# Kernel tuning notes

Hardware: AMD Instinct MI355X
Metric: run time of the kernel (lower is better)

## Reference

```python
import jax, jax.numpy as jnp
import numpy as np

N_NODES = 50000
N_EDGES = 800000
IN_DIM = 64
HID = 128
NUM_GRAPHS = 256


def setup_inputs() -> dict:
    key = jax.random.key(0)
    ks = jax.random.split(key, 20)
    inp = {
        'x': jax.random.normal(ks[0], (N_NODES, IN_DIM), dtype=jnp.float32),
        'edge_index': jax.random.randint(ks[1], (2, N_EDGES), 0, N_NODES, dtype=jnp.int32),
        'batch_idx': jnp.sort(jax.random.randint(ks[2], (N_NODES,), 0, NUM_GRAPHS, dtype=jnp.int32)),
    }
    # GIN layer MLP params (3 layers): Linear(in,hid)->ReLU->Linear(hid,hid)
    dims = [(IN_DIM, HID), (HID, HID), (HID, HID)]
    ki = 3
    for li, (di, dh) in enumerate(dims):
        s1 = 1.0 / np.sqrt(di)
        s2 = 1.0 / np.sqrt(dh)
        inp[f'gin{li}_w1'] = jax.random.uniform(ks[ki], (di, dh), jnp.float32, -s1, s1); ki += 1
        inp[f'gin{li}_b1'] = jnp.zeros((dh,), jnp.float32)
        inp[f'gin{li}_w2'] = jax.random.uniform(ks[ki], (dh, dh), jnp.float32, -s2, s2); ki += 1
        inp[f'gin{li}_b2'] = jnp.zeros((dh,), jnp.float32)
    # head: Linear(2*HID, HID) -> ReLU -> (Dropout eval=id) -> Linear(HID, 1)
    sh = 1.0 / np.sqrt(2 * HID)
    so = 1.0 / np.sqrt(HID)
    inp['head_w1'] = jax.random.uniform(ks[ki], (2 * HID, HID), jnp.float32, -sh, sh); ki += 1
    inp['head_b1'] = jnp.zeros((HID,), jnp.float32)
    inp['head_w2'] = jax.random.uniform(ks[ki], (HID, 1), jnp.float32, -so, so); ki += 1
    inp['head_b2'] = jnp.zeros((1,), jnp.float32)
    return inp


def _gin_layer(h, src, dst, w1, b1, w2, b2):
    # GINConv with eps=0: mlp(x + sum_{j->i} x_j), followed by outer ReLU
    agg = jax.ops.segment_sum(h[src], dst, num_segments=N_NODES)
    z = h + agg
    z = jnp.dot(jax.nn.relu(jnp.dot(z, w1) + b1), w2) + b2
    return jax.nn.relu(z)


def reference(x, edge_index, batch_idx,
              gin0_w1, gin0_b1, gin0_w2, gin0_b2,
              gin1_w1, gin1_b1, gin1_w2, gin1_b2,
              gin2_w1, gin2_b1, gin2_w2, gin2_b2,
              head_w1, head_b1, head_w2, head_b2):
    src, dst = edge_index[0], edge_index[1]
    h = _gin_layer(x, src, dst, gin0_w1, gin0_b1, gin0_w2, gin0_b2)
    h = _gin_layer(h, src, dst, gin1_w1, gin1_b1, gin1_w2, gin1_b2)
    h = _gin_layer(h, src, dst, gin2_w1, gin2_b1, gin2_w2, gin2_b2)
    # meanmax readout over graphs
    cnt = jax.ops.segment_sum(jnp.ones((h.shape[0],), h.dtype), batch_idx,
                              num_segments=NUM_GRAPHS)  # [G]
    ssum = jax.ops.segment_sum(h, batch_idx, num_segments=NUM_GRAPHS)  # [G, HID]
    mean_pool = ssum / jnp.maximum(cnt, 1.0)[:, None]
    max_pool = jax.ops.segment_max(h, batch_idx, num_segments=NUM_GRAPHS)
    max_pool = jnp.where(cnt[:, None] > 0, max_pool, 0.0)
    graph_repr = jnp.concatenate([mean_pool, max_pool], axis=-1)  # [G, 2*HID]
    # fraud head (dropout is identity in eval)
    hh = jax.nn.relu(jnp.dot(graph_repr, head_w1) + head_b1)
    logits = jnp.dot(hh, head_w2) + head_b2  # [G, 1]
    score = jax.nn.sigmoid(logits)
    return score
```

## Files before the change

kernel.cpp:

```cpp
#include <hip/hip_runtime.h>
#include <hip/hip_bf16.h>

#define N_NODES   50000
#define N_EDGES   800000
#define IN_DIM    64
#define HID       128
#define NUM_GRAPHS 256
#define NBUCK     196
#define BCAP      8192

typedef __bf16 bf16x8 __attribute__((ext_vector_type(8)));
typedef unsigned short u16x8 __attribute__((ext_vector_type(8)));
typedef float f32x4 __attribute__((ext_vector_type(4)));

__device__ __forceinline__ float b2f(unsigned short u) {
    return __uint_as_float(((unsigned int)u) << 16);
}
__device__ __forceinline__ unsigned short f2b(float f) {
    unsigned int x = __float_as_uint(f);
    x = (x + 0x7fffu + ((x >> 16) & 1u)) >> 16;
    return (unsigned short)x;
}

__global__ void diag_kernel(unsigned short* out, unsigned short pat) {
    out[threadIdx.x] = pat;
}

__global__ __launch_bounds__(256) void mega_pre_kernel(
    const unsigned short* __restrict__ x,
    const void* w0, const void* w1, const void* w2,
    const void* w3, const void* w4, const void* w5,
    unsigned short* __restrict__ wfbase,
    const int* __restrict__ batch, int* __restrict__ gstart,
    float* __restrict__ psum, unsigned int* __restrict__ pmax,
    const void* hw1, unsigned short* __restrict__ w1t,
    int* __restrict__ bcursor, int* __restrict__ flagp) {
    int b = blockIdx.x;
    int tid = threadIdx.x;

    if (b < 352) {
        __shared__ int cnt;
        if (tid == 0) cnt = 0;
        __syncthreads();
        unsigned short u = x[2 * tid];
        int e = (u >> 7) & 0xff;
        if (e <= 100 || e >= 140) atomicAdd(&cnt, 1);
        __syncthreads();
        int flag = cnt > 64;

        int mat, boff;
        if (b < 32) { mat = 0; boff = b; }
        else { mat = 1 + (b - 32) / 64; boff = (b - 32) % 64; }
        const void* W = mat == 0 ? w0 : mat == 1 ? w1 : mat == 2 ? w2
                      : mat == 3 ? w3 : mat == 4 ? w4 : w5;
        int KC = (mat == 0) ? 2 : 4;
        int idx = boff * 256 + tid;
        int j  = idx & 7;
        int l  = (idx >> 3) & 63;
        int tc = idx >> 9;
        int c  = tc % KC;
        int t  = tc / KC;
        int k  = c * 32 + (l >> 4) * 8 + j;
        int n  = t * 16 + (l & 15);
        unsigned short v = flag ? f2b(((const float*)W)[k * 128 + n])
                                : ((const unsigned short*)W)[k * 128 + n];
        wfbase[mat * 16384 + idx] = v;
    } else if (b < 548) {
        int i = (b - 352) * 256 + tid;
        if (i < NUM_GRAPHS * HID) { psum[i] = 0.0f; pmax[i] = 0u; }
        if (i >= N_NODES) return;
        int b1 = batch[i];
        int b0 = (i == 0) ? -1 : batch[i - 1];
        for (int g = b0 + 1; g <= b1; g++) gstart[g] = i;
        if (i == N_NODES - 1)
            for (int g = b1 + 1; g <= NUM_GRAPHS; g++) gstart[g] = N_NODES;
    } else if (b < 580) {
        __shared__ int cnt;
        if (tid == 0) cnt = 0;
        __syncthreads();
        unsigned short u = x[2 * tid];
        int e = (u >> 7) & 0xff;
        if (e <= 100 || e >= 140) atomicAdd(&cnt, 1);
        __syncthreads();
        int flag = cnt > 64;
        int base = (b - 548) * 1024;
#pragma unroll
        for (int j = 0; j < 4; j++) {
            int idx = base + j * 256 + tid;
            int n = idx >> 8;
            int k = idx & 255;
            unsigned short v = flag ? f2b(((const float*)hw1)[k * 128 + n])
                                    : ((const unsigned short*)hw1)[k * 128 + n];
            w1t[idx] = v;
        }
    } else {
        if (tid < NBUCK) bcursor[tid] = tid * BCAP;
        __shared__ int cnt;
        if (tid == 0) cnt = 0;
        __syncthreads();
        int c = 0;
        for (int j = 0; j < 16; j++) {
            unsigned short u = x[2 * (tid * 16 + j)];
            int e = (u >> 7) & 0xff;
            if (e <= 100 || e >= 140) c++;
        }
        atomicAdd(&cnt, c);
        __syncthreads();
        if (tid == 0) *flagp = (cnt > 1024) ? 1 : 0;
    }
}

__global__ __launch_bounds__(1024) void bscatter_kernel(const int* __restrict__ src,
        const int* __restrict__ dst, int* __restrict__ bcursor,
        unsigned int* __restrict__ ebuf) {
    __shared__ int lcnt[NBUCK];
    __shared__ int lbase[NBUCK];
    __shared__ int lcur[NBUCK];
    int tid = threadIdx.x;
    if (tid < NBUCK) lcnt[tid] = 0;
    __syncthreads();
    int e0 = blockIdx.x * 4096;
    int d[4], s[4];
#pragma unroll
    for (int k = 0; k < 4; k++) {
        int e = e0 + k * 1024 + tid;
        if (e < N_EDGES) {
            d[k] = dst[e]; s[k] = src[e];
            atomicAdd(&lcnt[d[k] >> 8], 1);
        } else d[k] = -1;
    }
    __syncthreads();
    if (tid < NBUCK) {
        int c = lcnt[tid];
        lbase[tid] = c ? atomicAdd(&bcursor[tid], c) : 0;
        lcur[tid] = 0;
    }
    __syncthreads();
#pragma unroll
    for (int k = 0; k < 4; k++) {
        if (d[k] >= 0) {
            int b = d[k] >> 8;
            int p = lbase[b] + atomicAdd(&lcur[b], 1);
            ebuf[p] = ((unsigned int)(d[k] & 255) << 16) | (unsigned int)s[k];
        }
    }
}

__global__ __launch_bounds__(256) void bsort_kernel(const unsigned int* __restrict__ ebuf,
        const int* __restrict__ bcursor, int* __restrict__ off,
        unsigned short* __restrict__ csr) {
    __shared__ int cntA[256];
    __shared__ int sc[256];
    __shared__ int lcnt[256];
    __shared__ int lcur[256];
    int b = blockIdx.x, tid = threadIdx.x;

    int v = (tid < NBUCK) ? (bcursor[tid] - tid * BCAP) : 0;
    cntA[tid] = v;
    sc[tid] = v;
    __syncthreads();
    for (int d = 1; d < 256; d <<= 1) {
        int t = (tid >= d) ? sc[tid - d] : 0;
        __syncthreads();
        sc[tid] += t;
        __syncthreads();
    }
    int base = sc[b] - cntA[b];
    int cnt  = cntA[b];
    int ebase = b * BCAP;
    __syncthreads();

    lcnt[tid] = 0;
    __syncthreads();
    for (int i = tid; i < cnt; i += 256)
        atomicAdd(&lcnt[ebuf[ebase + i] >> 16], 1);
    __syncthreads();
    int v2 = lcnt[tid];
    sc[tid] = v2;
    __syncthreads();
    for (int d = 1; d < 256; d <<= 1) {
        int t = (tid >= d) ? sc[tid - d] : 0;
        __syncthreads();
        sc[tid] += t;
        __syncthreads();
    }
    int excl = sc[tid] - v2;
    lcur[tid] = excl;
    int node = b * 256 + tid;
    if (node < N_NODES) off[node] = base + excl;
    if (b == 0 && tid == 0) off[N_NODES] = N_EDGES;
    __syncthreads();
    for (int i = tid; i < cnt; i += 256) {
        unsigned int ev = ebuf[ebase + i];
        int p = atomicAdd(&lcur[ev >> 16], 1);
        csr[base + p] = (unsigned short)(ev & 0xffffu);
    }
}

template <int K1, bool POOL, bool FROMX>
__global__ __launch_bounds__(256, 3) void fused_gin_kernel(
    const void* __restrict__ X,
    const int* __restrict__ off, const unsigned short* __restrict__ csr,
    const unsigned short* __restrict__ Wf1, const void* __restrict__ bias1,
    const unsigned short* __restrict__ Wf2, const void* __restrict__ bias2,
    unsigned short* __restrict__ Out, int M, const int* __restrict__ flagp,
    const int* __restrict__ batch, float* __restrict__ psum,
    unsigned int* __restrict__ pmax) {
    constexpr int KC1 = K1 / 32;
    __shared__ __align__(16) unsigned short lds_hi[64 * 136];
    __shared__ __align__(16) unsigned short lds_lo[64 * 136];
    __shared__ int batch_lds[64];

    int flag = *flagp;
    int wave = threadIdx.x >> 6;
    int lane = threadIdx.x & 63;
    int m_ = lane & 15;
    int q  = lane >> 4;

    if constexpr (POOL) {
        if (threadIdx.x < 64) {
            int gr = blockIdx.x * 64 + threadIdx.x;
            batch_lds[threadIdx.x] = gr < M ? batch[gr] : -1;
        }
    }

    int np = lane >> 4;
    int l  = lane & 15;
#pragma unroll 1
    for (int p = 0; p < 4; p++) {
        int nl = wave * 16 + p * 4 + np;
        int node = blockIdx.x * 64 + nl;
        int nodec = node < M ? node : (M - 1);
        int s = off[nodec], e = off[nodec + 1];
        if constexpr (FROMX) {
            float a0, a1, a2, a3;
            float b0 = 0.f, b1 = 0.f, b2 = 0.f, b3 = 0.f;
            float c0 = 0.f, c1 = 0.f, c2 = 0.f, c3 = 0.f;
            float d0 = 0.f, d1 = 0.f, d2 = 0.f, d3 = 0.f;
            if (flag) {
                const float4* xp = (const float4*)X;
                float4 u = xp[(size_t)nodec * 16 + l];
                a0 = u.x; a1 = u.y; a2 = u.z; a3 = u.w;
                int i = s;
                for (; i + 3 < e; i += 4) {
                    float4 v0 = xp[(size_t)csr[i] * 16 + l];
                    float4 v1 = xp[(size_t)csr[i + 1] * 16 + l];
                    float4 v2 = xp[(size_t)csr[i + 2] * 16 + l];
                    float4 v3 = xp[(size_t)csr[i + 3] * 16 + l];
                    a0 += v0.x; a1 += v0.y; a2 += v0.z; a3 += v0.w;
                    b0 += v1.x; b1 += v1.y; b2 += v1.z; b3 += v1.w;
                    c0 += v2.x; c1 += v2.y; c2 += v2.z; c3 += v2.w;
                    d0 += v3.x; d1 += v3.y; d2 += v3.z; d3 += v3.w;
                }
                for (; i < e; i++) {
                    float4 v = xp[(size_t)csr[i] * 16 + l];
                    a0 += v.x; a1 += v.y; a2 += v.z; a3 += v.w;
                }
            } else {
                const ushort4* xp = (const ushort4*)X;
                ushort4 u = xp[(size_t)nodec * 16 + l];
                a0 = b2f(u.x); a1 = b2f(u.y); a2 = b2f(u.z); a3 = b2f(u.w);
                int i = s;
                for (; i + 3 < e; i += 4) {
                    ushort4 v0 = xp[(size_t)csr[i] * 16 + l];
                    ushort4 v1 = xp[(size_t)csr[i + 1] * 16 + l];
                    ushort4 v2 = xp[(size_t)csr[i + 2] * 16 + l];
                    ushort4 v3 = xp[(size_t)csr[i + 3] * 16 + l];
                    a0 += b2f(v0.x); a1 += b2f(v0.y); a2 += b2f(v0.z); a3 += b2f(v0.w);
                    b0 += b2f(v1.x); b1 += b2f(v1.y); b2 += b2f(v1.z); b3 += b2f(v1.w);
                    c0 += b2f(v2.x); c1 += b2f(v2.y); c2 += b2f(v2.z); c3 += b2f(v2.w);
                    d0 += b2f(v3.x); d1 += b2f(v3.y); d2 += b2f(v3.z); d3 += b2f(v3.w);
                }
                for (; i < e; i++) {
                    ushort4 v = xp[(size_t)csr[i] * 16 + l];
                    a0 += b2f(v.x); a1 += b2f(v.y); a2 += b2f(v.z); a3 += b2f(v.w);
                }
            }
            ushort4 o;
            o.x = f2b(a0 + b0 + c0 + d0);
            o.y = f2b(a1 + b1 + c1 + d1);
            o.z = f2b(a2 + b2 + c2 + d2);
            o.w = f2b(a3 + b3 + c3 + d3);
            *reinterpret_cast<ushort4*>(&lds_hi[nl * 136 + l * 4]) = o;
        } else {
            const u16x8* hp = (const u16x8*)X;
            u16x8 u = hp[(size_t)nodec * 16 + l];
            float a[8], b[8], c[8], d[8];
#pragma unroll
            for (int j = 0; j < 8; j++) { a[j] = b2f(u[j]); b[j] = 0.f; c[j] = 0.f; d[j] = 0.f; }
            int i = s;
            for (; i + 3 < e; i += 4) {
                u16x8 v0 = hp[(size_t)csr[i] * 16 + l];
                u16x8 v1 = hp[(size_t)csr[i + 1] * 16 + l];
                u16x8 v2 = hp[(size_t)csr[i + 2] * 16 + l];
                u16x8 v3 = hp[(size_t)csr[i + 3] * 16 + l];
#pragma unroll
                for (int j = 0; j < 8; j++) {
                    a[j] += b2f(v0[j]); b[j] += b2f(v1[j]);
                    c[j] += b2f(v2[j]); d[j] += b2f(v3[j]);
                }
            }
            for (; i < e; i++) {
                u16x8 v = hp[(size_t)csr[i] * 16 + l];
#pragma unroll
                for (int j = 0; j < 8; j++) a[j] += b2f(v[j]);
            }
            u16x8 o;
#pragma unroll
            for (int j = 0; j < 8; j++) o[j] = f2b(a[j] + b[j] + c[j] + d[j]);
            *reinterpret_cast<u16x8*>(&lds_hi[nl * 136 + l * 8]) = o;
        }
    }

    const unsigned short* wfl1 = Wf1 + lane * 8;
    const unsigned short* wfl2 = Wf2 + lane * 8;
    const unsigned short* zlds = &lds_hi[(wave * 16 + m_) * 136 + q * 8];

    bf16x8 afrag[KC1];
#pragma unroll
    for (int c = 0; c < KC1; c++)
        afrag[c] = *reinterpret_cast<const bf16x8*>(zlds + c * 32);

    float b1v[8], b2v[8];
#pragma unroll
    for (int t = 0; t < 8; t++) {
        int col = t * 16 + m_;
        b1v[t] = flag ? ((const float*)bias1)[col]
                      : b2f(((const unsigned short*)bias1)[col]);
        b2v[t] = flag ? ((const float*)bias2)[col]
                      : b2f(((const unsigned short*)bias2)[col]);
    }

    f32x4 acc[8];
#pragma unroll
    for (int t = 0; t < 8; t++) acc[t] = (f32x4)(0.0f);

    {
        bf16x8 wb[8], wn[8];
#pragma unroll
        for (int t = 0; t < 8; t++)
            wb[t] = *reinterpret_cast<const bf16x8*>(wfl1 + ((t * KC1 + 0) << 9));
#pragma unroll
        for (int c = 0; c < KC1; c++) {
            if (c + 1 < KC1) {
#pragma unroll
                for (int t = 0; t < 8; t++)
                    wn[t] = *reinterpret_cast<const bf16x8*>(wfl1 + ((t * KC1 + c + 1) << 9));
            }
#pragma unroll
            for (int t = 0; t < 8; t++)
                acc[t] = __builtin_amdgcn_mfma_f32_16x16x32_bf16(afrag[c], wb[t], acc[t], 0, 0, 0);
            if (c + 1 < KC1) {
#pragma unroll
                for (int t = 0; t < 8; t++) wb[t] = wn[t];
            }
        }
    }

#pragma unroll
    for (int r = 0; r < 4; r++) {
        int lr = wave * 16 + q * 4 + r;
#pragma unroll
        for (int t = 0; t < 8; t++) {
            int col = t * 16 + m_;
            float v = acc[t][r] + b1v[t];
            v = v > 0.0f ? v : 0.0f;
            unsigned short hb = f2b(v);
            lds_hi[lr * 136 + col] = hb;
            lds_lo[lr * 136 + col] = f2b(v - b2f(hb));
        }
    }

#pragma unroll
    for (int t = 0; t < 8; t++) acc[t] = (f32x4)(0.0f);

    {
        int lr2 = wave * 16 + m_;
        const unsigned short* hibase = &lds_hi[lr2 * 136 + q * 8];
        const unsigned short* lobase = &lds_lo[lr2 * 136 + q * 8];
        bf16x8 wb[8], wn[8];
#pragma unroll
        for (int t = 0; t < 8; t++)
            wb[t] = *reinterpret_cast<const bf16x8*>(wfl2 + ((t * 4 + 0) << 9));
#pragma unroll
        for (int c = 0; c < 4; c++) {
            if (c < 3) {
#pragma unroll
                for (int t = 0; t < 8; t++)
                    wn[t] = *reinterpret_cast<const bf16x8*>(wfl2 + ((t * 4 + c + 1) << 9));
            }
            bf16x8 ahi = *reinterpret_cast<const bf16x8*>(hibase + c * 32);
            bf16x8 alo = *reinterpret_cast<const bf16x8*>(lobase + c * 32);
#pragma unroll
            for (int t = 0; t < 8; t++) {
                acc[t] = __builtin_amdgcn_mfma_f32_16x16x32_bf16(ahi, wb[t], acc[t], 0, 0, 0);
                acc[t] = __builtin_amdgcn_mfma_f32_16x16x32_bf16(alo, wb[t], acc[t], 0, 0, 0);
            }
            if (c < 3) {
#pragma unroll
                for (int t = 0; t < 8; t++) wb[t] = wn[t];
            }
        }
    }

#pragma unroll
    for (int r = 0; r < 4; r++) {
        int lr = wave * 16 + q * 4 + r;
        int orow = blockIdx.x * 64 + lr;
#pragma unroll
        for (int t = 0; t < 8; t++) {
            int col = t * 16 + m_;
            float v = acc[t][r] + b2v[t];
            v = v > 0.0f ? v : 0.0f;
            if constexpr (POOL) {
                lds_hi[lr * 136 + col] = f2b(v);
            } else {
                if (orow < M) Out[(size_t)orow * HID + col] = f2b(v);
            }
        }
    }

    if constexpr (POOL) {
        __syncthreads();
        int f = threadIdx.x;
        if (f < HID) {
            int cur = -1;
            float sum = 0.0f, mx = 0.0f;
            for (int rrow = 0; rrow < 64; rrow++) {
                int g = batch_lds[rrow];
                if (g < 0) break;
                float v = b2f(lds_hi[rrow * 136 + f]);
                if (g == cur) {
                    sum += v;
                    mx = fmaxf(mx, v);
                } else {
                    if (cur >= 0) {
                        atomicAdd(&psum[cur * HID + f], sum);
                        atomicMax(&pmax[cur * HID + f], __float_as_uint(mx));
                    }
                    cur = g; sum = v; mx = v;
                }
            }
            if (cur >= 0) {
                atomicAdd(&psum[cur * HID + f], sum);
                atomicMax(&pmax[cur * HID + f], __float_as_uint(mx));
            }
        }
    }
}

__global__ __launch_bounds__(128) void head_kernel(
    const float* __restrict__ psum, const unsigned int* __restrict__ pmax,
    const int* __restrict__ gstart,
    const unsigned short* __restrict__ w1t,
    const void* __restrict__ b1, const void* __restrict__ w2,
    const void* __restrict__ b2,
    void* __restrict__ out, const int* __restrict__ flagp) {
    int g = blockIdx.x;
    int n = threadIdx.x;
    int flag = *flagp;
    __shared__ float repr[2 * HID];
    __shared__ float red[HID];

    float c = (float)(gstart[g + 1] - gstart[g]);
    float inv = 1.0f / fmaxf(c, 1.0f);
    repr[n]       = psum[g * HID + n] * inv;
    repr[HID + n] = __uint_as_float(pmax[g * HID + n]);
    __syncthreads();

    const u16x8* wp = (const u16x8*)(w1t + n * 256);
    float a0 = 0.f, a1 = 0.f, a2 = 0.f, a3 = 0.f;
#pragma unroll
    for (int c8 = 0; c8 < 32; c8 += 4) {
        u16x8 w0 = wp[c8 + 0];
        u16x8 w1 = wp[c8 + 1];
        u16x8 w2v = wp[c8 + 2];
        u16x8 w3 = wp[c8 + 3];
#pragma unroll
        for (int j = 0; j < 8; j++) {
            a0 += repr[(c8 + 0) * 8 + j] * b2f(w0[j]);
            a1 += repr[(c8 + 1) * 8 + j] * b2f(w1[j]);
            a2 += repr[(c8 + 2) * 8 + j] * b2f(w2v[j]);
            a3 += repr[(c8 + 3) * 8 + j] * b2f(w3[j]);
        }
    }
    float b1v = flag ? ((const float*)b1)[n] : b2f(((const unsigned short*)b1)[n]);
    float acc = a0 + a1 + a2 + a3 + b1v;
    acc = fmaxf(acc, 0.0f);

    float w2s = flag ? ((const float*)w2)[n] : b2f(((const unsigned short*)w2)[n]);
    red[n] = acc * w2s;
    __syncthreads();
    for (int s = 64; s > 0; s >>= 1) {
        if (n < s) red[n] += red[n + s];
        __syncthreads();
    }
    if (n == 0) {
        float b2v = flag ? ((const float*)b2)[0] : b2f(((const unsigned short*)b2)[0]);
        float logit = red[0] + b2v;
        float sv = 1.0f / (1.0f + expf(-logit));
        if (flag) ((float*)out)[g] = sv;
        else      ((unsigned short*)out)[g] = f2b(sv);
    }
}

extern "C" void kernel_launch(void* const* d_in, const int* in_sizes, int n_in,
                              void* d_out, int out_size, void* d_ws, size_t ws_size,
                              hipStream_t stream) {
    const int* edge = (const int*)d_in[1];
    const int* srcv = edge;
    const int* dstv = edge + N_EDGES;
    const int* batch = (const int*)d_in[2];

    char* ws = (char*)d_ws;
    unsigned short* A = (unsigned short*)ws;
    unsigned short* B = (unsigned short*)(ws + 12800000);
    unsigned int* ebuf = (unsigned int*)(ws + 25600000);
    unsigned short* csr = (unsigned short*)(ws + 32100000);
    int* off    = (int*)(ws + 33700000);
    unsigned short* wfbase = (unsigned short*)(ws + 33904000);
    float* psum  = (float*)(ws + 34100608);
    unsigned int* pmax = (unsigned int*)(ws + 34231680);
    int* bcursor = (int*)(ws + 34362752);
    int* gstart  = (int*)(ws + 34363776);
    int* flagp   = (int*)(ws + 34365824);
    unsigned short* w1t = (unsigned short*)(ws + 34366848);

    const size_t NEED = 34500000;
    if (ws_size < NEED) {
        unsigned int k = 0;
        while ((((size_t)1) << (k + 1)) <= ws_size && k < 62) k++;
        diag_kernel<<<1, 256, 0, stream>>>((unsigned short*)d_out,
                                           (unsigned short)(0x4000 | (k & 63)));
        return;
    }

    mega_pre_kernel<<<581, 256, 0, stream>>>(
        (const unsigned short*)d_in[0],
        d_in[3], d_in[5], d_in[7], d_in[9], d_in[11], d_in[13], wfbase,
        batch, gstart, psum, pmax, d_in[15], w1t, bcursor, flagp);

    const int EB = (N_EDGES + 4095) / 4096;
    bscatter_kernel<<<EB, 1024, 0, stream>>>(srcv, dstv, bcursor, ebuf);
    bsort_kernel<<<NBUCK, 256, 0, stream>>>(ebuf, bcursor, off, csr);

    const int GEMM_GRID = (N_NODES + 63) / 64;

    fused_gin_kernel<64, false, true><<<GEMM_GRID, 256, 0, stream>>>(
        d_in[0], off, csr,
        wfbase + 0 * 16384, d_in[4], wfbase + 1 * 16384, d_in[6],
        A, N_NODES, flagp, batch, psum, pmax);

    fused_gin_kernel<128, false, false><<<GEMM_GRID, 256, 0, stream>>>(
        A, off, csr,
        wfbase + 2 * 16384, d_in[8], wfbase + 3 * 16384, d_in[10],
        B, N_NODES, flagp, batch, psum, pmax);

    fused_gin_kernel<128, true, false><<<GEMM_GRID, 256, 0, stream>>>(
        B, off, csr,
        wfbase + 4 * 16384, d_in[12], wfbase + 5 * 16384, d_in[14],
        A , N_NODES, flagp, batch, psum, pmax);

    head_kernel<<<NUM_GRAPHS, 128, 0, stream>>>(psum, pmax, gstart, w1t,
                                                d_in[16], d_in[17], d_in[18],
                                                d_out, flagp);
}
```

Baseline: 254.7 us.

## Use 8 waves per GIN block, splitting rows and output columns across waves

Doubles the block to 512 threads so each wave gathers 8 nodes instead of 16. In both MLP GEMMs each wave now computes a 16-row by 64-column tile, with waves split by row and column half. A separate z_lds buffer and block-wide barriers are added because waves now share LDS rows. The aim is more latency hiding for the irregular neighbour gather and lower per-wave register pressure. The cost is extra LDS per block, more barriers, and weight fragments reloaded by twice as many waves.

Result: slower. 276.0 us (+8.4%).

```diff
diff --git a/kernel.cpp b/kernel.cpp
--- a/kernel.cpp
+++ b/kernel.cpp
@@ -198,7 +198,7 @@
 }
 
 template <int K1, bool POOL, bool FROMX>
-__global__ __launch_bounds__(256, 3) void fused_gin_kernel(
+__global__ __launch_bounds__(512, 6) void fused_gin_kernel(
     const void* __restrict__ X,
     const int* __restrict__ off, const unsigned short* __restrict__ csr,
     const unsigned short* __restrict__ Wf1, const void* __restrict__ bias1,
@@ -207,6 +207,7 @@
     const int* __restrict__ batch, float* __restrict__ psum,
     unsigned int* __restrict__ pmax) {
     constexpr int KC1 = K1 / 32;
+    __shared__ __align__(16) unsigned short z_lds[64 * 136];
     __shared__ __align__(16) unsigned short lds_hi[64 * 136];
     __shared__ __align__(16) unsigned short lds_lo[64 * 136];
     __shared__ int batch_lds[64];
@@ -216,6 +217,8 @@
     int lane = threadIdx.x & 63;
     int m_ = lane & 15;
     int q  = lane >> 4;
+    int wr = wave >> 1;
+    int wc = wave & 1;
 
     if constexpr (POOL) {
         if (threadIdx.x < 64) {
@@ -227,8 +230,8 @@
     int np = lane >> 4;
     int l  = lane & 15;
 #pragma unroll 1
-    for (int p = 0; p < 4; p++) {
-        int nl = wave * 16 + p * 4 + np;
+    for (int p = 0; p < 2; p++) {
+        int nl = wave * 8 + p * 4 + np;
         int node = blockIdx.x * 64 + nl;
         int nodec = node < M ? node : (M - 1);
         int s = off[nodec], e = off[nodec + 1];
@@ -281,7 +284,7 @@
             o.y = f2b(a1 + b1 + c1 + d1);
             o.z = f2b(a2 + b2 + c2 + d2);
             o.w = f2b(a3 + b3 + c3 + d3);
-            *reinterpret_cast<ushort4*>(&lds_hi[nl * 136 + l * 4]) = o;
+            *reinterpret_cast<ushort4*>(&z_lds[nl * 136 + l * 4]) = o;
         } else {
             const u16x8* hp = (const u16x8*)X;
             u16x8 u = hp[(size_t)nodec * 16 + l];
@@ -308,61 +311,62 @@
             u16x8 o;
 #pragma unroll
             for (int j = 0; j < 8; j++) o[j] = f2b(a[j] + b[j] + c[j] + d[j]);
-            *reinterpret_cast<u16x8*>(&lds_hi[nl * 136 + l * 8]) = o;
-        }
-    }
+            *reinterpret_cast<u16x8*>(&z_lds[nl * 136 + l * 8]) = o;
+        }
+    }
+    __syncthreads();
 
     const unsigned short* wfl1 = Wf1 + lane * 8;
     const unsigned short* wfl2 = Wf2 + lane * 8;
-    const unsigned short* zlds = &lds_hi[(wave * 16 + m_) * 136 + q * 8];
+    const unsigned short* zp = &z_lds[(wr * 16 + m_) * 136 + q * 8];
 
     bf16x8 afrag[KC1];
 #pragma unroll
     for (int c = 0; c < KC1; c++)
-        afrag[c] = *reinterpret_cast<const bf16x8*>(zlds + c * 32);
-
-    float b1v[8], b2v[8];
-#pragma unroll
-    for (int t = 0; t < 8; t++) {
-        int col = t * 16 + m_;
+        afrag[c] = *reinterpret_cast<const bf16x8*>(zp + c * 32);
+
+    float b1v[4], b2v[4];
+#pragma unroll
+    for (int t = 0; t < 4; t++) {
+        int col = (wc * 4 + t) * 16 + m_;
         b1v[t] = flag ? ((const float*)bias1)[col]
                       : b2f(((const unsigned short*)bias1)[col]);
         b2v[t] = flag ? ((const float*)bias2)[col]
                       : b2f(((const unsigned short*)bias2)[col]);
     }
 
-    f32x4 acc[8];
-#pragma unroll
-    for (int t = 0; t < 8; t++) acc[t] = (f32x4)(0.0f);
+    f32x4 acc[4];
+#pragma unroll
+    for (int t = 0; t < 4; t++) acc[t] = (f32x4)(0.0f);
 
     {
-        bf16x8 wb[8], wn[8];
-#pragma unroll
-        for (int t = 0; t < 8; t++)
-            wb[t] = *reinterpret_cast<const bf16x8*>(wfl1 + ((t * KC1 + 0) << 9));
+        bf16x8 wb[4], wn[4];
+#pragma unroll
+        for (int t = 0; t < 4; t++)
+            wb[t] = *reinterpret_cast<const bf16x8*>(wfl1 + (((wc * 4 + t) * KC1 + 0) << 9));
 #pragma unroll
         for (int c = 0; c < KC1; c++) {
             if (c + 1 < KC1) {
 #pragma unroll
-                for (int t = 0; t < 8; t++)
-                    wn[t] = *reinterpret_cast<const bf16x8*>(wfl1 + ((t * KC1 + c + 1) << 9));
-            }
-#pragma unroll
-            for (int t = 0; t < 8; t++)
+                for (int t = 0; t < 4; t++)
+                    wn[t] = *reinterpret_cast<const bf16x8*>(wfl1 + (((wc * 4 + t) * KC1 + c + 1) << 9));
+            }
+#pragma unroll
+            for (int t = 0; t < 4; t++)
                 acc[t] = __builtin_amdgcn_mfma_f32_16x16x32_bf16(afrag[c], wb[t], acc[t], 0, 0, 0);
             if (c + 1 < KC1) {
 #pragma unroll
-                for (int t = 0; t < 8; t++) wb[t] = wn[t];
+                for (int t = 0; t < 4; t++) wb[t] = wn[t];
             }
         }
     }
 
 #pragma unroll
     for (int r = 0; r < 4; r++) {
-        int lr = wave * 16 + q * 4 + r;
-#pragma unroll
-        for (int t = 0; t < 8; t++) {
-            int col = t * 16 + m_;
+        int lr = wr * 16 + q * 4 + r;
+#pragma unroll
+        for (int t = 0; t < 4; t++) {
+            int col = (wc * 4 + t) * 16 + m_;
             float v = acc[t][r] + b1v[t];
             v = v > 0.0f ? v : 0.0f;
             unsigned short hb = f2b(v);
@@ -370,46 +374,50 @@
             lds_lo[lr * 136 + col] = f2b(v - b2f(hb));
         }
     }
-
-#pragma unroll
-    for (int t = 0; t < 8; t++) acc[t] = (f32x4)(0.0f);
+    __syncthreads();
+
+#pragma unroll
+    for (int t = 0; t < 4; t++) acc[t] = (f32x4)(0.0f);
 
     {
-        int lr2 = wave * 16 + m_;
+        int lr2 = wr * 16 + m_;
         const unsigned short* hibase = &lds_hi[lr2 * 136 + q * 8];
         const unsigned short* lobase = &lds_lo[lr2 * 136 + q * 8];
-        bf16x8 wb[8], wn[8];
-#pragma unroll
-        for (int t = 0; t < 8; t++)
-            wb[t] = *reinterpret_cast<const bf16x8*>(wfl2 + ((t * 4 + 0) << 9));
+        bf16x8 wb[4], wn[4];
+#pragma unroll
+        for (int t = 0; t < 4; t++)
+            wb[t] = *reinterpret_cast<const bf16x8*>(wfl2 + (((wc * 4 + t) * 4 + 0) << 9));
 #pragma unroll
         for (int c = 0; c < 4; c++) {
             if (c < 3) {
 #pragma unroll
-                for (int t = 0; t < 8; t++)
-                    wn[t] = *reinterpret_cast<const bf16x8*>(wfl2 + ((t * 4 + c + 1) << 9));
+                for (int t = 0; t < 4; t++)
+                    wn[t] = *reinterpret_cast<const bf16x8*>(wfl2 + (((wc * 4 + t) * 4 + c + 1) << 9));
             }
             bf16x8 ahi = *reinterpret_cast<const bf16x8*>(hibase + c * 32);
             bf16x8 alo = *reinterpret_cast<const bf16x8*>(lobase + c * 32);
 #pragma unroll
-            for (int t = 0; t < 8; t++) {
+            for (int t = 0; t < 4; t++) {
                 acc[t] = __builtin_amdgcn_mfma_f32_16x16x32_bf16(ahi, wb[t], acc[t], 0, 0, 0);
                 acc[t] = __builtin_amdgcn_mfma_f32_16x16x32_bf16(alo, wb[t], acc[t], 0, 0, 0);
             }
             if (c < 3) {
 #pragma unroll
-                for (int t = 0; t < 8; t++) wb[t] = wn[t];
-            }
-        }
-    }
-
+                for (int t = 0; t < 4; t++) wb[t] = wn[t];
+            }
+        }
+    }
+
+    if constexpr (POOL) {
+        __syncthreads();
+    }
 #pragma unroll
     for (int r = 0; r < 4; r++) {
-        int lr = wave * 16 + q * 4 + r;
+        int lr = wr * 16 + q * 4 + r;
         int orow = blockIdx.x * 64 + lr;
 #pragma unroll
-        for (int t = 0; t < 8; t++) {
-            int col = t * 16 + m_;
+        for (int t = 0; t < 4; t++) {
+            int col = (wc * 4 + t) * 16 + m_;
             float v = acc[t][r] + b2v[t];
             v = v > 0.0f ? v : 0.0f;
             if constexpr (POOL) {
@@ -546,17 +554,17 @@
 
     const int GEMM_GRID = (N_NODES + 63) / 64;
 
-    fused_gin_kernel<64, false, true><<<GEMM_GRID, 256, 0, stream>>>(
+    fused_gin_kernel<64, false, true><<<GEMM_GRID, 512, 0, stream>>>(
         d_in[0], off, csr,
         wfbase + 0 * 16384, d_in[4], wfbase + 1 * 16384, d_in[6],
         A, N_NODES, flagp, batch, psum, pmax);
 
-    fused_gin_kernel<128, false, false><<<GEMM_GRID, 256, 0, stream>>>(
+    fused_gin_kernel<128, false, false><<<GEMM_GRID, 512, 0, stream>>>(
         A, off, csr,
         wfbase + 2 * 16384, d_in[8], wfbase + 3 * 16384, d_in[10],
         B, N_NODES, flagp, batch, psum, pmax);
 
-    fused_gin_kernel<128, true, false><<<GEMM_GRID, 256, 0, stream>>>(
+    fused_gin_kernel<128, true, false><<<GEMM_GRID, 512, 0, stream>>>(
         B, off, csr,
         wfbase + 4 * 16384, d_in[12], wfbase + 5 * 16384, d_in[14],
         A , N_NODES, flagp, batch, psum, pmax);
```

## Replace bucketed scatter-sort CSR build with degree-count, scan, atomic scatter

Applied to the files above, without the earlier changes.

Builds the dst-sorted CSR with a plain counting sort: a per-node degree histogram via global atomics, a two-level prefix scan (block partial sums, then offsets), and a scatter using per-node atomic cursors. This removes the intermediate 32-bit edge bucket buffer and the per-bucket LDS sort pass. In exchange it adds two kernel launches, and both edge passes use contended global atomics. Edge order within each node's neighbour list becomes nondeterministic, which can reorder the float accumulation in the aggregation.

Result: slower. 310.6 us (+21.9%).

```diff
diff --git a/kernel.cpp b/kernel.cpp
--- a/kernel.cpp
+++ b/kernel.cpp
@@ -7,7 +7,6 @@
 #define HID       128
 #define NUM_GRAPHS 256
 #define NBUCK     196
-#define BCAP      8192
 
 typedef __bf16 bf16x8 __attribute__((ext_vector_type(8)));
 typedef unsigned short u16x8 __attribute__((ext_vector_type(8)));
@@ -34,7 +33,7 @@
     const int* __restrict__ batch, int* __restrict__ gstart,
     float* __restrict__ psum, unsigned int* __restrict__ pmax,
     const void* hw1, unsigned short* __restrict__ w1t,
-    int* __restrict__ bcursor, int* __restrict__ flagp) {
+    int* __restrict__ deg, int* __restrict__ flagp) {
     int b = blockIdx.x;
     int tid = threadIdx.x;
 
@@ -68,6 +67,7 @@
     } else if (b < 548) {
         int i = (b - 352) * 256 + tid;
         if (i < NUM_GRAPHS * HID) { psum[i] = 0.0f; pmax[i] = 0u; }
+        deg[i] = 0;
         if (i >= N_NODES) return;
         int b1 = batch[i];
         int b0 = (i == 0) ? -1 : batch[i - 1];
@@ -94,7 +94,6 @@
             w1t[idx] = v;
         }
     } else {
-        if (tid < NBUCK) bcursor[tid] = tid * BCAP;
         __shared__ int cnt;
         if (tid == 0) cnt = 0;
         __syncthreads();
@@ -110,90 +109,62 @@
     }
 }
 
-__global__ __launch_bounds__(1024) void bscatter_kernel(const int* __restrict__ src,
-        const int* __restrict__ dst, int* __restrict__ bcursor,
-        unsigned int* __restrict__ ebuf) {
-    __shared__ int lcnt[NBUCK];
-    __shared__ int lbase[NBUCK];
-    __shared__ int lcur[NBUCK];
-    int tid = threadIdx.x;
-    if (tid < NBUCK) lcnt[tid] = 0;
+__global__ __launch_bounds__(1024) void deg_kernel(const int* __restrict__ dst,
+        int* __restrict__ deg) {
+    int e = blockIdx.x * 1024 + threadIdx.x;
+    if (e < N_EDGES) atomicAdd(&deg[dst[e]], 1);
+}
+
+__global__ __launch_bounds__(256) void part_kernel(const int* __restrict__ deg,
+        int* __restrict__ part) {
+    __shared__ int red[256];
+    int b = blockIdx.x, t = threadIdx.x;
+    red[t] = deg[b * 256 + t];
     __syncthreads();
-    int e0 = blockIdx.x * 4096;
-    int d[4], s[4];
-#pragma unroll
-    for (int k = 0; k < 4; k++) {
-        int e = e0 + k * 1024 + tid;
-        if (e < N_EDGES) {
-            d[k] = dst[e]; s[k] = src[e];
-            atomicAdd(&lcnt[d[k] >> 8], 1);
-        } else d[k] = -1;
-    }
-    __syncthreads();
-    if (tid < NBUCK) {
-        int c = lcnt[tid];
-        lbase[tid] = c ? atomicAdd(&bcursor[tid], c) : 0;
-        lcur[tid] = 0;
-    }
-    __syncthreads();
-#pragma unroll
-    for (int k = 0; k < 4; k++) {
-        if (d[k] >= 0) {
-            int b = d[k] >> 8;
-            int p = lbase[b] + atomicAdd(&lcur[b], 1);
-            ebuf[p] = ((unsigned int)(d[k] & 255) << 16) | (unsigned int)s[k];
-        }
-    }
-}
-
-__global__ __launch_bounds__(256) void bsort_kernel(const unsigned int* __restrict__ ebuf,
-        const int* __restrict__ bcursor, int* __restrict__ off,
-        unsigned short* __restrict__ csr) {
-    __shared__ int cntA[256];
+    for (int s = 128; s > 0; s >>= 1) {
+        if (t < s) red[t] += red[t + s];
+        __syncthreads();
+    }
+    if (t == 0) part[b] = red[0];
+}
+
+__global__ __launch_bounds__(256) void off_kernel(const int* __restrict__ deg,
+        const int* __restrict__ part, int* __restrict__ off, int* __restrict__ cur) {
     __shared__ int sc[256];
-    __shared__ int lcnt[256];
-    __shared__ int lcur[256];
-    int b = blockIdx.x, tid = threadIdx.x;
-
-    int v = (tid < NBUCK) ? (bcursor[tid] - tid * BCAP) : 0;
-    cntA[tid] = v;
-    sc[tid] = v;
+    __shared__ int ls[256];
+    int b = blockIdx.x, t = threadIdx.x;
+    sc[t] = (t < NBUCK) ? part[t] : 0;
     __syncthreads();
     for (int d = 1; d < 256; d <<= 1) {
-        int t = (tid >= d) ? sc[tid - d] : 0;
-        __syncthreads();
-        sc[tid] += t;
-        __syncthreads();
-    }
-    int base = sc[b] - cntA[b];
-    int cnt  = cntA[b];
-    int ebase = b * BCAP;
-    __syncthreads();
-
-    lcnt[tid] = 0;
-    __syncthreads();
-    for (int i = tid; i < cnt; i += 256)
-        atomicAdd(&lcnt[ebuf[ebase + i] >> 16], 1);
-    __syncthreads();
-    int v2 = lcnt[tid];
-    sc[tid] = v2;
+        int v = (t >= d) ? sc[t - d] : 0;
+        __syncthreads();
+        sc[t] += v;
+        __syncthreads();
+    }
+    int base = (b == 0) ? 0 : sc[b - 1];
+    int dv = deg[b * 256 + t];
+    ls[t] = dv;
     __syncthreads();
     for (int d = 1; d < 256; d <<= 1) {
-        int t = (tid >= d) ? sc[tid - d] : 0;
-        __syncthreads();
-        sc[tid] += t;
-        __syncthreads();
-    }
-    int excl = sc[tid] - v2;
-    lcur[tid] = excl;
-    int node = b * 256 + tid;
-    if (node < N_NODES) off[node] = base + excl;
-    if (b == 0 && tid == 0) off[N_NODES] = N_EDGES;
-    __syncthreads();
-    for (int i = tid; i < cnt; i += 256) {
-        unsigned int ev = ebuf[ebase + i];
-        int p = atomicAdd(&lcur[ev >> 16], 1);
-        csr[base + p] = (unsigned short)(ev & 0xffffu);
+        int v = (t >= d) ? ls[t - d] : 0;
+        __syncthreads();
+        ls[t] += v;
+        __syncthreads();
+    }
+    int node = b * 256 + t;
+    int o = base + ls[t] - dv;
+    if (node < N_NODES) { off[node] = o; cur[node] = o; }
+    if (b == 0 && t == 0) off[N_NODES] = N_EDGES;
+}
+
+__global__ __launch_bounds__(1024) void scatter_kernel(const int* __restrict__ src,
+        const int* __restrict__ dst, int* __restrict__ cur,
+        unsigned short* __restrict__ csr) {
+    int e = blockIdx.x * 1024 + threadIdx.x;
+    if (e < N_EDGES) {
+        int d = dst[e];
+        int p = atomicAdd(&cur[d], 1);
+        csr[p] = (unsigned short)src[e];
     }
 }
 
@@ -515,13 +486,14 @@
     char* ws = (char*)d_ws;
     unsigned short* A = (unsigned short*)ws;
     unsigned short* B = (unsigned short*)(ws + 12800000);
-    unsigned int* ebuf = (unsigned int*)(ws + 25600000);
+    int* deg  = (int*)(ws + 25600000);
+    int* part = (int*)(ws + 25800704);
+    int* cur  = (int*)(ws + 25801728);
     unsigned short* csr = (unsigned short*)(ws + 32100000);
     int* off    = (int*)(ws + 33700000);
     unsigned short* wfbase = (unsigned short*)(ws + 33904000);
     float* psum  = (float*)(ws + 34100608);
     unsigned int* pmax = (unsigned int*)(ws + 34231680);
-    int* bcursor = (int*)(ws + 34362752);
     int* gstart  = (int*)(ws + 34363776);
     int* flagp   = (int*)(ws + 34365824);
     unsigned short* w1t = (unsigned short*)(ws + 34366848);
@@ -538,11 +510,13 @@
     mega_pre_kernel<<<581, 256, 0, stream>>>(
         (const unsigned short*)d_in[0],
         d_in[3], d_in[5], d_in[7], d_in[9], d_in[11], d_in[13], wfbase,
-        batch, gstart, psum, pmax, d_in[15], w1t, bcursor, flagp);
-
-    const int EB = (N_EDGES + 4095) / 4096;
-    bscatter_kernel<<<EB, 1024, 0, stream>>>(srcv, dstv, bcursor, ebuf);
-    bsort_kernel<<<NBUCK, 256, 0, stream>>>(ebuf, bcursor, off, csr);
+        batch, gstart, psum, pmax, d_in[15], w1t, deg, flagp);
+
+    const int EB = (N_EDGES + 1023) / 1024;
+    deg_kernel<<<EB, 1024, 0, stream>>>(dstv, deg);
+    part_kernel<<<NBUCK, 256, 0, stream>>>(deg, part);
+    off_kernel<<<NBUCK, 256, 0, stream>>>(deg, part, off, cur);
+    scatter_kernel<<<EB, 1024, 0, stream>>>(srcv, dstv, cur, csr);
 
     const int GEMM_GRID = (N_NODES + 63) / 64;
 
```

## Shrink fused GIN blocks to a single wave of 16 nodes

Applied to the files above, without the earlier changes.

Each fused GIN kernel now launches 64-thread blocks covering 16 nodes each, where before it used 256-thread blocks covering 64 nodes. The aim is a smaller LDS footprint per block, finer-grained scheduling to absorb uneven node degrees, and no idle waves waiting at block barriers. Because 50000 divides evenly by 16, the bounds checks and index clamping are removed. In exchange there are four times as many blocks, and per-block work such as bias and weight loads and pooling atomics (now once per 16 rows instead of once per 64) is repeated more often.

New measurement: 261.4 us. 1.03x slower.

```diff
diff --git a/kernel.cpp b/kernel.cpp
--- a/kernel.cpp
+++ b/kernel.cpp
@@ -198,7 +198,7 @@
 }
 
 template <int K1, bool POOL, bool FROMX>
-__global__ __launch_bounds__(256, 3) void fused_gin_kernel(
+__global__ __launch_bounds__(64, 6) void fused_gin_kernel(
     const void* __restrict__ X,
     const int* __restrict__ off, const unsigned short* __restrict__ csr,
     const unsigned short* __restrict__ Wf1, const void* __restrict__ bias1,
@@ -207,31 +207,26 @@
     const int* __restrict__ batch, float* __restrict__ psum,
     unsigned int* __restrict__ pmax) {
     constexpr int KC1 = K1 / 32;
-    __shared__ __align__(16) unsigned short lds_hi[64 * 136];
-    __shared__ __align__(16) unsigned short lds_lo[64 * 136];
-    __shared__ int batch_lds[64];
+    __shared__ __align__(16) unsigned short lds_hi[16 * 136];
+    __shared__ __align__(16) unsigned short lds_lo[16 * 136];
+    __shared__ int batch_lds[16];
 
     int flag = *flagp;
-    int wave = threadIdx.x >> 6;
-    int lane = threadIdx.x & 63;
+    int lane = threadIdx.x;
     int m_ = lane & 15;
     int q  = lane >> 4;
 
     if constexpr (POOL) {
-        if (threadIdx.x < 64) {
-            int gr = blockIdx.x * 64 + threadIdx.x;
-            batch_lds[threadIdx.x] = gr < M ? batch[gr] : -1;
-        }
+        if (lane < 16) batch_lds[lane] = batch[blockIdx.x * 16 + lane];
     }
 
     int np = lane >> 4;
     int l  = lane & 15;
 #pragma unroll 1
     for (int p = 0; p < 4; p++) {
-        int nl = wave * 16 + p * 4 + np;
-        int node = blockIdx.x * 64 + nl;
-        int nodec = node < M ? node : (M - 1);
-        int s = off[nodec], e = off[nodec + 1];
+        int nl = p * 4 + np;
+        int node = blockIdx.x * 16 + nl;
+        int s = off[node], e = off[node + 1];
         if constexpr (FROMX) {
             float a0, a1, a2, a3;
             float b0 = 0.f, b1 = 0.f, b2 = 0.f, b3 = 0.f;
@@ -239,7 +234,7 @@
             float d0 = 0.f, d1 = 0.f, d2 = 0.f, d3 = 0.f;
             if (flag) {
                 const float4* xp = (const float4*)X;
-                float4 u = xp[(size_t)nodec * 16 + l];
+                float4 u = xp[(size_t)node * 16 + l];
                 a0 = u.x; a1 = u.y; a2 = u.z; a3 = u.w;
                 int i = s;
                 for (; i + 3 < e; i += 4) {
@@ -258,7 +253,7 @@
                 }
             } else {
                 const ushort4* xp = (const ushort4*)X;
-                ushort4 u = xp[(size_t)nodec * 16 + l];
+                ushort4 u = xp[(size_t)node * 16 + l];
                 a0 = b2f(u.x); a1 = b2f(u.y); a2 = b2f(u.z); a3 = b2f(u.w);
                 int i = s;
                 for (; i + 3 < e; i += 4) {
@@ -284,7 +279,7 @@
             *reinterpret_cast<ushort4*>(&lds_hi[nl * 136 + l * 4]) = o;
         } else {
             const u16x8* hp = (const u16x8*)X;
-            u16x8 u = hp[(size_t)nodec * 16 + l];
+            u16x8 u = hp[(size_t)node * 16 + l];
             float a[8], b[8], c[8], d[8];
 #pragma unroll
             for (int j = 0; j < 8; j++) { a[j] = b2f(u[j]); b[j] = 0.f; c[j] = 0.f; d[j] = 0.f; }
@@ -314,7 +309,7 @@
 
     const unsigned short* wfl1 = Wf1 + lane * 8;
     const unsigned short* wfl2 = Wf2 + lane * 8;
-    const unsigned short* zlds = &lds_hi[(wave * 16 + m_) * 136 + q * 8];
+    const unsigned short* zlds = &lds_hi[m_ * 136 + q * 8];
 
     bf16x8 afrag[KC1];
 #pragma unroll
@@ -359,7 +354,7 @@
 
 #pragma unroll
     for (int r = 0; r < 4; r++) {
-        int lr = wave * 16 + q * 4 + r;
+        int lr = q * 4 + r;
 #pragma unroll
         for (int t = 0; t < 8; t++) {
             int col = t * 16 + m_;
@@ -375,9 +370,8 @@
     for (int t = 0; t < 8; t++) acc[t] = (f32x4)(0.0f);
 
     {
-        int lr2 = wave * 16 + m_;
-        const unsigned short* hibase = &lds_hi[lr2 * 136 + q * 8];
-        const unsigned short* lobase = &lds_lo[lr2 * 136 + q * 8];
+        const unsigned short* hibase = &lds_hi[m_ * 136 + q * 8];
+        const unsigned short* lobase = &lds_lo[m_ * 136 + q * 8];
         bf16x8 wb[8], wn[8];
 #pragma unroll
         for (int t = 0; t < 8; t++)
@@ -405,8 +399,8 @@
 
 #pragma unroll
     for (int r = 0; r < 4; r++) {
-        int lr = wave * 16 + q * 4 + r;
-        int orow = blockIdx.x * 64 + lr;
+        int lr = q * 4 + r;
+        int orow = blockIdx.x * 16 + lr;
 #pragma unroll
         for (int t = 0; t < 8; t++) {
             int col = t * 16 + m_;
@@ -415,20 +409,18 @@
             if constexpr (POOL) {
                 lds_hi[lr * 136 + col] = f2b(v);
             } else {
-                if (orow < M) Out[(size_t)orow * HID + col] = f2b(v);
+                Out[(size_t)orow * HID + col] = f2b(v);
             }
         }
     }
 
     if constexpr (POOL) {
         __syncthreads();
-        int f = threadIdx.x;
-        if (f < HID) {
+        for (int f = lane; f < HID; f += 64) {
             int cur = -1;
             float sum = 0.0f, mx = 0.0f;
-            for (int rrow = 0; rrow < 64; rrow++) {
+            for (int rrow = 0; rrow < 16; rrow++) {
                 int g = batch_lds[rrow];
-                if (g < 0) break;
                 float v = b2f(lds_hi[rrow * 136 + f]);
                 if (g == cur) {
                     sum += v;
@@ -544,19 +536,19 @@
     bscatter_kernel<<<EB, 1024, 0, stream>>>(srcv, dstv, bcursor, ebuf);
     bsort_kernel<<<NBUCK, 256, 0, stream>>>(ebuf, bcursor, off, csr);
 
-    const int GEMM_GRID = (N_NODES + 63) / 64;
-
-    fused_gin_kernel<64, false, true><<<GEMM_GRID, 256, 0, stream>>>(
+    const int GIN_GRID = N_NODES / 16;
+
+    fused_gin_kernel<64, false, true><<<GIN_GRID, 64, 0, stream>>>(
         d_in[0], off, csr,
         wfbase + 0 * 16384, d_in[4], wfbase + 1 * 16384, d_in[6],
         A, N_NODES, flagp, batch, psum, pmax);
 
-    fused_gin_kernel<128, false, false><<<GEMM_GRID, 256, 0, stream>>>(
+    fused_gin_kernel<128, false, false><<<GIN_GRID, 64, 0, stream>>>(
         A, off, csr,
         wfbase + 2 * 16384, d_in[8], wfbase + 3 * 16384, d_in[10],
         B, N_NODES, flagp, batch, psum, pmax);
 
-    fused_gin_kernel<128, true, false><<<GEMM_GRID, 256, 0, stream>>>(
+    fused_gin_kernel<128, true, false><<<GIN_GRID, 64, 0, stream>>>(
         B, off, csr,
         wfbase + 4 * 16384, d_in[12], wfbase + 5 * 16384, d_in[14],
         A , N_NODES, flagp, batch, psum, pmax);
```
